# Kernel tuning notes

Measured on AMD Instinct MI355X. Metric: run time of the kernel, lower is better.

## Reference

```python
import jax, jax.numpy as jnp
import numpy as np
import math

D_MODEL = 1024
N_HEAD = 16


def setup_inputs() -> dict:
    key = jax.random.key(0)
    ks = jax.random.split(key, 11)
    B, S, D = 2, 2048, D_MODEL
    s = 1.0 / math.sqrt(D)
    return {
        "q": jax.random.normal(ks[0], (B, S, D), dtype=jnp.float32),
        "k": jax.random.normal(ks[1], (B, S, D), dtype=jnp.float32),
        "v": jax.random.normal(ks[2], (B, S, D), dtype=jnp.float32),
        "w_q": jax.random.normal(ks[3], (D, D), dtype=jnp.float32) * s,
        "b_q": jnp.zeros((D,), dtype=jnp.float32),
        "w_k": jax.random.normal(ks[4], (D, D), dtype=jnp.float32) * s,
        "b_k": jnp.zeros((D,), dtype=jnp.float32),
        "w_v": jax.random.normal(ks[5], (D, D), dtype=jnp.float32) * s,
        "b_v": jnp.zeros((D,), dtype=jnp.float32),
        "w_out": jax.random.normal(ks[6], (D, D), dtype=jnp.float32) * s,
        "b_out": jnp.zeros((D,), dtype=jnp.float32),
    }


def _split_heads(x, n_head):
    B, S, D = x.shape
    return x.reshape(B, S, n_head, D // n_head).transpose(0, 2, 1, 3)  # [B,H,S,dk]


def reference(q, k, v, w_q, b_q, w_k, b_k, w_v, b_v, w_out, b_out):
    # Linear projections (weights stored as [in, out])
    qh = _split_heads(q @ w_q + b_q, N_HEAD)
    kh = _split_heads(k @ w_k + b_k, N_HEAD)
    vh = _split_heads(v @ w_v + b_v, N_HEAD)
    d_k = qh.shape[-1]
    scores = jnp.einsum("bhqd,bhkd->bhqk", qh, kh) / jnp.sqrt(jnp.float32(d_k))
    attn = jax.nn.softmax(scores, axis=-1)
    context = jnp.einsum("bhqk,bhkd->bhqd", attn, vh)  # [B,H,S,dk]
    B, H, S, dk = context.shape
    context = context.transpose(0, 2, 1, 3).reshape(B, S, H * dk)
    return context @ w_out + b_out
```

## Files before the change

### kernel.cpp

```cpp
#include <hip/hip_runtime.h>
#include <hip/hip_bf16.h>


typedef __bf16 bf16x8 __attribute__((ext_vector_type(8)));
typedef float  f32x4  __attribute__((ext_vector_type(4)));

#define DEVI __device__ __forceinline__
#define SWZ(row, cb) ((cb) ^ (((row) & 7) << 4))

#define GLOAD16(gsrc, ldst)                                                    \
    __builtin_amdgcn_global_load_lds(                                          \
        (const __attribute__((address_space(1))) unsigned int*)(gsrc),         \
        (__attribute__((address_space(3))) unsigned int*)(ldst), 16, 0, 0)

#define BAR()        asm volatile("s_barrier" ::: "memory")
#define WAIT_LGKM0() asm volatile("s_waitcnt lgkmcnt(0)" ::: "memory")
#define WAIT_VM0()   asm volatile("s_waitcnt vmcnt(0)" ::: "memory")
#define WAIT_VM4()   asm volatile("s_waitcnt vmcnt(4)" ::: "memory")

static DEVI unsigned short f2bf(float f) {
    __hip_bfloat16 h = __float2bfloat16(f);
    return __builtin_bit_cast(unsigned short, h);
}
static DEVI unsigned int pack2(float a, float b) {
    return (unsigned int)f2bf(a) | ((unsigned int)f2bf(b) << 16);
}
static DEVI bf16x8 ldsRead(const char* p) {
    return __builtin_bit_cast(bf16x8, *(const uint4*)p);
}

__global__ __launch_bounds__(256) void wtrans_kernel(
    const float* w0, const float* w1, const float* w2, const float* w3,
    unsigned short* t0, unsigned short* t1, unsigned short* t2, unsigned short* t3)
{
    __shared__ unsigned short tile[64][80];
    const int z = blockIdx.z;
    const float* w = (z == 0) ? w0 : (z == 1) ? w1 : (z == 2) ? w2 : w3;
    unsigned short* wt = (z == 0) ? t0 : (z == 1) ? t1 : (z == 2) ? t2 : t3;
    const int n0 = blockIdx.x * 64, k0 = blockIdx.y * 64;
    const int t = threadIdx.x;
#pragma unroll
    for (int i = 0; i < 4; i++) {
        int chunk = t + i * 256;
        int row = chunk >> 4, c4 = chunk & 15;
        float4 v = *(const float4*)(w + (size_t)(k0 + row) * 1024 + n0 + c4 * 4);
        tile[c4 * 4 + 0][row] = f2bf(v.x);
        tile[c4 * 4 + 1][row] = f2bf(v.y);
        tile[c4 * 4 + 2][row] = f2bf(v.z);
        tile[c4 * 4 + 3][row] = f2bf(v.w);
    }
    __syncthreads();
#pragma unroll
    for (int i = 0; i < 2; i++) {
        int idx = t + i * 256;
        int row = idx >> 3, ch = idx & 7;
        uint4 vv = *(const uint4*)(&tile[row][ch * 8]);
        *(uint4*)(wt + (size_t)(n0 + row) * 1024 + k0 + ch * 8) = vv;
    }
}

__global__ __launch_bounds__(256, 3) void gemm_proj_kernel(
    const float* x0, const float* x1, const float* x2,
    const unsigned short* wt0, const unsigned short* wt1, const unsigned short* wt2,
    const float* b0, const float* b1, const float* b2,
    unsigned short* y0, unsigned short* y1, unsigned short* y2)
{
    __shared__ __align__(16) char Af[32768];
    __shared__ __align__(16) char Bs[16384];
    const int i = blockIdx.x;
    const int xcd = i & 7, j = i >> 3;
    const int panel = xcd * 12 + (j >> 3);
    const int z = panel >> 5, mblk = panel & 31;
    const int n0 = (j & 7) * 128, m0 = mblk * 128;

    const float* X = (z == 0) ? x0 : (z == 1) ? x1 : x2;
    const unsigned short* Wt = (z == 0) ? wt0 : (z == 1) ? wt1 : wt2;
    const float* bias = (z == 0) ? b0 : (z == 1) ? b1 : b2;
    unsigned short* Y = (z == 0) ? y0 : (z == 1) ? y1 : y2;
    const float scale = (z == 0) ? 0.125f * 1.44269504f : 1.0f;
    const int t = threadIdx.x, w = t >> 6, l = t & 63, l15 = l & 15, l4 = l >> 4;
    const int wr = w >> 1, wc = w & 1;
    const char* Ab = (const char*)X;
    const char* Bb = (const char*)Wt;

    f32x4 acc[4][4];
#pragma unroll
    for (int mr = 0; mr < 4; mr++)
#pragma unroll
        for (int nc = 0; nc < 4; nc++) acc[mr][nc] = f32x4{0.f, 0.f, 0.f, 0.f};

#pragma unroll 1
    for (int k = 0; k < 16; ++k) {
        const int k0 = k * 64;
        BAR();
#pragma unroll
        for (int jj = 0; jj < 8; jj++) {
            int o = w * 8192 + jj * 1024 + l * 16;
            int row = o >> 8, cb = (o >> 4) & 15;
            int csw = cb ^ ((row & 7) << 1);
            GLOAD16(Ab + ((size_t)(m0 + row) * 1024 + k0 + csw * 4) * 4,
                    Af + w * 8192 + jj * 1024);
        }
#pragma unroll
        for (int jj = 0; jj < 4; jj++) {
            int o = w * 4096 + jj * 1024 + l * 16;
            int row = o >> 7, cb = (o >> 4) & 7;
            int csw = cb ^ (row & 7);
            GLOAD16(Bb + ((size_t)(n0 + row) * 1024 + k0 + csw * 8) * 2,
                    Bs + w * 4096 + jj * 1024);
        }
        WAIT_VM0();
        BAR();

        bf16x8 af[4][2], bfr[4][2];
#pragma unroll
        for (int mr = 0; mr < 4; mr++) {
            int row = wr * 64 + mr * 16 + l15;
            int x = (row & 7) << 1;
#pragma unroll
            for (int kf = 0; kf < 2; kf++) {
                int cb = kf * 8 + l4 * 2;
                const char* p = Af + row * 256 + (cb ^ x) * 16;
                float4 a = *(const float4*)p;
                float4 b = *(const float4*)(p + 16);
                uint4 pk = {pack2(a.x, a.y), pack2(a.z, a.w),
                            pack2(b.x, b.y), pack2(b.z, b.w)};
                af[mr][kf] = __builtin_bit_cast(bf16x8, pk);
            }
        }
#pragma unroll
        for (int nc = 0; nc < 4; nc++) {
            int row = wc * 64 + nc * 16 + l15;
#pragma unroll
            for (int kf = 0; kf < 2; kf++)
                bfr[nc][kf] = ldsRead(Bs + row * 128 + SWZ(row, kf * 64 + l4 * 16));
        }
        __builtin_amdgcn_s_setprio(1);
#pragma unroll
        for (int kf = 0; kf < 2; kf++)
#pragma unroll
            for (int mr = 0; mr < 4; mr++)
#pragma unroll
                for (int nc = 0; nc < 4; nc++)
                    acc[mr][nc] = __builtin_amdgcn_mfma_f32_16x16x32_bf16(
                        af[mr][kf], bfr[nc][kf], acc[mr][nc], 0, 0, 0);
        __builtin_amdgcn_s_setprio(0);
    }

    WAIT_LGKM0();
    BAR();
    char* Es = Af;
    if (z < 2) {
#pragma unroll
        for (int nc = 0; nc < 4; nc++) {
            float bv = bias[n0 + wc * 64 + nc * 16 + l15];
#pragma unroll
            for (int mr = 0; mr < 4; mr++)
#pragma unroll
                for (int r = 0; r < 4; r++) {
                    int mloc = wr * 64 + mr * 16 + l4 * 4 + r;
                    int nloc = wc * 64 + nc * 16 + l15;
                    *(unsigned short*)(Es + mloc * 256 + nloc * 2) =
                        f2bf((acc[mr][nc][r] + bv) * scale);
                }
        }
        WAIT_LGKM0();
        BAR();
#pragma unroll
        for (int ii = 0; ii < 8; ii++) {
            int idx = t + ii * 256, row = idx >> 4, ch = idx & 15;
            *(uint4*)((char*)Y + ((size_t)(m0 + row) * 1024 + n0 + ch * 8) * 2) =
                *(const uint4*)(Es + row * 256 + ch * 16);
        }
    } else {
#pragma unroll
        for (int nc = 0; nc < 4; nc++) {
            float bv = bias[n0 + wc * 64 + nc * 16 + l15];
#pragma unroll
            for (int mr = 0; mr < 4; mr++)
#pragma unroll
                for (int r = 0; r < 4; r++) {
                    int mloc = wr * 64 + mr * 16 + l4 * 4 + r;
                    int nloc = wc * 64 + nc * 16 + l15;
                    *(unsigned short*)(Es + nloc * 256 + mloc * 2) =
                        f2bf(acc[mr][nc][r] + bv);
                }
        }
        WAIT_LGKM0();
        BAR();
        const int bb = m0 >> 11, s0 = m0 & 2047;
#pragma unroll
        for (int ii = 0; ii < 8; ii++) {
            int idx = t + ii * 256, row = idx >> 4, ch = idx & 15;
            int col = n0 + row, h = col >> 6, d = col & 63;
            *(uint4*)((char*)Y +
                      (((size_t)((bb * 16 + h) * 64 + d)) * 2048 + s0 + ch * 8) * 2) =
                *(const uint4*)(Es + row * 256 + ch * 16);
        }
    }
}

__global__ __launch_bounds__(256, 4) void attn_kernel(
    const unsigned short* Q2, const unsigned short* K2, const unsigned short* VT,
    unsigned short* ctx)
{
    __shared__ __align__(16) char sm[40960];
    char* QPs = sm;
    char* K0s = sm + 8192;
    char* K1s = sm + 16384;
    char* V0s = sm + 24576;
    char* V1s = sm + 32768;
    const int t = threadIdx.x, w = t >> 6, l = t & 63, l15 = l & 15, l4 = l >> 4;
    char* Ps = QPs + w * 2048;

    const int i = blockIdx.x;
    const int xcd = i & 7, j = i >> 3;
    const int bh = xcd * 4 + (j >> 5), qblk = j & 31;
    const int b = bh >> 4, h = bh & 15;
    const int q0 = qblk * 64;
    const int t0 = qblk;
    const char* Qb = (const char*)(Q2 + ((size_t)(b * 2048 + q0)) * 1024 + h * 64);
    const char* Kb = (const char*)(K2 + ((size_t)(b * 2048)) * 1024 + h * 64);
    const char* Vb = (const char*)(VT + (size_t)bh * 64 * 2048);

    int kGO[2], vGO[2];
#pragma unroll
    for (int jj = 0; jj < 2; jj++) {
        int row = w * 16 + jj * 8 + (l >> 3);
        int ch = (l & 7) ^ (row & 7);
        kGO[jj] = row * 2048 + ch * 16;
        vGO[jj] = row * 4096 + ch * 16;
    }
    int kRO[4][2], vRO[4][2];
#pragma unroll
    for (int cc = 0; cc < 4; cc++) {
        int row = cc * 16 + l15;
#pragma unroll
        for (int kf = 0; kf < 2; kf++) {
            kRO[cc][kf] = row * 128 + SWZ(row, kf * 64 + l4 * 16);
            vRO[cc][kf] = kRO[cc][kf];
        }
    }
    int pWO[4], pRO[2];
#pragma unroll
    for (int cc = 0; cc < 4; cc++) {
        int c = (cc * 2 + (l4 >> 1)) ^ (l15 & 7);
        pWO[cc] = l15 * 128 + c * 16 + (l4 & 1) * 8;
    }
#pragma unroll
    for (int kf = 0; kf < 2; kf++)
        pRO[kf] = l15 * 128 + SWZ(l15, kf * 64 + l4 * 16);

#define STAGE_KV(TT, Kdst, Vdst)                                               \
    do {                                                                       \
        int kk0 = (TT) * 64;                                                   \
        _Pragma("unroll") for (int jj = 0; jj < 2; jj++) {                     \
            GLOAD16(Kb + (size_t)(kk0 * 2048 + kGO[jj]),                       \
                    (Kdst) + w * 2048 + jj * 1024);                            \
            GLOAD16(Vb + (size_t)(kk0 * 2 + vGO[jj]),                          \
                    (Vdst) + w * 2048 + jj * 1024);                            \
        }                                                                      \
    } while (0)

    STAGE_KV(t0, K0s, V0s);

#pragma unroll
    for (int ii = 0; ii < 2; ii++) {
        int idx = t + ii * 256, row = idx >> 3, ch = idx & 7;
        uint4 vv = *(const uint4*)(Qb + (size_t)row * 2048 + ch * 16);
        *(uint4*)(QPs + row * 128 + SWZ(row, ch * 16)) = vv;
    }
    WAIT_LGKM0();
    BAR();
    bf16x8 qf[2];
    {
        int row = w * 16 + l15;
#pragma unroll
        for (int kf = 0; kf < 2; kf++)
            qf[kf] = ldsRead(QPs + row * 128 + SWZ(row, kf * 64 + l4 * 16));
    }
    WAIT_LGKM0();
    BAR();

    bf16x8 ones;
#pragma unroll
    for (int e = 0; e < 8; e++) ones[e] = (__bf16)1.0f;

    f32x4 o[4], ol;
#pragma unroll
    for (int c = 0; c < 4; c++) o[c] = f32x4{0.f, 0.f, 0.f, 0.f};
    ol = f32x4{0.f, 0.f, 0.f, 0.f};

#pragma unroll 1
    for (int it = 0; it < 32; it++) {
        char* Kc = (it & 1) ? K1s : K0s;
        char* Vc = (it & 1) ? V1s : V0s;
        char* Kn = (it & 1) ? K0s : K1s;
        char* Vn = (it & 1) ? V0s : V1s;
        if (it < 31) {
            STAGE_KV((t0 + it + 1) & 31, Kn, Vn);
            WAIT_VM4();
        } else {
            WAIT_VM0();
        }
        BAR();

        f32x4 sacc[4];
#pragma unroll
        for (int c = 0; c < 4; c++) sacc[c] = f32x4{0.f, 0.f, 0.f, 0.f};
        __builtin_amdgcn_s_setprio(1);
#pragma unroll
        for (int cc = 0; cc < 4; cc++)
#pragma unroll
            for (int kf = 0; kf < 2; kf++) {
                bf16x8 kfrag = ldsRead(Kc + kRO[cc][kf]);
                sacc[cc] = __builtin_amdgcn_mfma_f32_16x16x32_bf16(kfrag, qf[kf], sacc[cc], 0, 0, 0);
            }
        __builtin_amdgcn_s_setprio(0);

#pragma unroll
        for (int cc = 0; cc < 4; cc++)
#pragma unroll
            for (int r = 0; r < 4; r++) sacc[cc][r] = exp2f(sacc[cc][r]);

#pragma unroll
        for (int cc = 0; cc < 4; cc++) {
            uint2 pk = {pack2(sacc[cc][0], sacc[cc][1]), pack2(sacc[cc][2], sacc[cc][3])};
            *(uint2*)(Ps + pWO[cc]) = pk;
        }
        asm volatile("" ::: "memory");
        bf16x8 pf[2];
#pragma unroll
        for (int kf = 0; kf < 2; kf++)
            pf[kf] = ldsRead(Ps + pRO[kf]);

        __builtin_amdgcn_s_setprio(1);
#pragma unroll
        for (int dd = 0; dd < 4; dd++)
#pragma unroll
            for (int kf = 0; kf < 2; kf++) {
                bf16x8 vfrag = ldsRead(Vc + vRO[dd][kf]);
                o[dd] = __builtin_amdgcn_mfma_f32_16x16x32_bf16(vfrag, pf[kf], o[dd], 0, 0, 0);
            }
#pragma unroll
        for (int kf = 0; kf < 2; kf++)
            ol = __builtin_amdgcn_mfma_f32_16x16x32_bf16(ones, pf[kf], ol, 0, 0, 0);
        __builtin_amdgcn_s_setprio(0);

        WAIT_LGKM0();
        BAR();
    }
#undef STAGE_KV

    float rinv = 1.0f / ol[0];
    int q = q0 + w * 16 + l15;
    unsigned short* crow = ctx + ((size_t)(b * 2048 + q)) * 1024 + h * 64;
#pragma unroll
    for (int dd = 0; dd < 4; dd++) {
        uint2 pk = {pack2(o[dd][0] * rinv, o[dd][1] * rinv),
                    pack2(o[dd][2] * rinv, o[dd][3] * rinv)};
        *(uint2*)(crow + dd * 16 + l4 * 4) = pk;
    }
}

__global__ __launch_bounds__(256, 3) void gemm_out_kernel(
    const unsigned short* ctx, const unsigned short* wto, const float* bias, float* out)
{
    __shared__ __align__(16) char As[16384];
    __shared__ __align__(16) char Bs[16384];
    const int i = blockIdx.x;
    const int xcd = i & 7, j = i >> 3;
    const int mpanel = xcd * 4 + (j >> 3);
    const int n0 = (j & 7) * 128, m0 = mpanel * 128;
    const int t = threadIdx.x, w = t >> 6, l = t & 63, l15 = l & 15, l4 = l >> 4;
    const int wr = w >> 1, wc = w & 1;
    const char* Ab = (const char*)ctx;
    const char* Bb = (const char*)wto;

    f32x4 acc[4][4];
#pragma unroll
    for (int mr = 0; mr < 4; mr++)
#pragma unroll
        for (int nc = 0; nc < 4; nc++) acc[mr][nc] = f32x4{0.f, 0.f, 0.f, 0.f};

#pragma unroll 1
    for (int k = 0; k < 16; ++k) {
        const int k0 = k * 64;
        BAR();
#pragma unroll
        for (int jj = 0; jj < 4; jj++) {
            int o = w * 4096 + jj * 1024 + l * 16;
            int row = o >> 7, cb = (o >> 4) & 7;
            int csw = cb ^ (row & 7);
            GLOAD16(Ab + ((size_t)(m0 + row) * 1024 + k0 + csw * 8) * 2,
                    As + w * 4096 + jj * 1024);
        }
#pragma unroll
        for (int jj = 0; jj < 4; jj++) {
            int o = w * 4096 + jj * 1024 + l * 16;
            int row = o >> 7, cb = (o >> 4) & 7;
            int csw = cb ^ (row & 7);
            GLOAD16(Bb + ((size_t)(n0 + row) * 1024 + k0 + csw * 8) * 2,
                    Bs + w * 4096 + jj * 1024);
        }
        WAIT_VM0();
        BAR();

        bf16x8 af[4][2], bfr[4][2];
#pragma unroll
        for (int mr = 0; mr < 4; mr++) {
            int row = wr * 64 + mr * 16 + l15;
#pragma unroll
            for (int kf = 0; kf < 2; kf++)
                af[mr][kf] = ldsRead(As + row * 128 + SWZ(row, kf * 64 + l4 * 16));
        }
#pragma unroll
        for (int nc = 0; nc < 4; nc++) {
            int row = wc * 64 + nc * 16 + l15;
#pragma unroll
            for (int kf = 0; kf < 2; kf++)
                bfr[nc][kf] = ldsRead(Bs + row * 128 + SWZ(row, kf * 64 + l4 * 16));
        }
        __builtin_amdgcn_s_setprio(1);
#pragma unroll
        for (int kf = 0; kf < 2; kf++)
#pragma unroll
            for (int mr = 0; mr < 4; mr++)
#pragma unroll
                for (int nc = 0; nc < 4; nc++)
                    acc[mr][nc] = __builtin_amdgcn_mfma_f32_16x16x32_bf16(
                        af[mr][kf], bfr[nc][kf], acc[mr][nc], 0, 0, 0);
        __builtin_amdgcn_s_setprio(0);
    }

#pragma unroll
    for (int nc = 0; nc < 4; nc++) {
        int col = n0 + wc * 64 + nc * 16 + l15;
        float bv = bias[col];
#pragma unroll
        for (int mr = 0; mr < 4; mr++)
#pragma unroll
            for (int r = 0; r < 4; r++) {
                int m = m0 + wr * 64 + mr * 16 + l4 * 4 + r;
                out[(size_t)m * 1024 + col] = acc[mr][nc][r] + bv;
            }
    }
}

extern "C" void kernel_launch(void* const* d_in, const int* in_sizes, int n_in,
                              void* d_out, int out_size, void* d_ws, size_t ws_size,
                              hipStream_t stream)
{
    (void)in_sizes; (void)n_in; (void)out_size; (void)ws_size;
    const float* q  = (const float*)d_in[0];
    const float* k  = (const float*)d_in[1];
    const float* v  = (const float*)d_in[2];
    const float* wq = (const float*)d_in[3];
    const float* bq = (const float*)d_in[4];
    const float* wk = (const float*)d_in[5];
    const float* bk = (const float*)d_in[6];
    const float* wv = (const float*)d_in[7];
    const float* bv = (const float*)d_in[8];
    const float* wo = (const float*)d_in[9];
    const float* bo = (const float*)d_in[10];

    char* ws = (char*)d_ws;
    const size_t MB = 1u << 20;
    unsigned short* WTq = (unsigned short*)(ws + 0 * MB);
    unsigned short* WTk = (unsigned short*)(ws + 2 * MB);
    unsigned short* WTv = (unsigned short*)(ws + 4 * MB);
    unsigned short* WTo = (unsigned short*)(ws + 6 * MB);
    unsigned short* Q2  = (unsigned short*)(ws + 8 * MB);
    unsigned short* K2  = (unsigned short*)(ws + 16 * MB);
    unsigned short* VT  = (unsigned short*)(ws + 24 * MB);
    unsigned short* CTX = (unsigned short*)(ws + 32 * MB);

    wtrans_kernel<<<dim3(16, 16, 4), 256, 0, stream>>>(wq, wk, wv, wo, WTq, WTk, WTv, WTo);
    gemm_proj_kernel<<<768, 256, 0, stream>>>(q, k, v, WTq, WTk, WTv,
                                              bq, bk, bv, Q2, K2, VT);
    attn_kernel<<<1024, 256, 0, stream>>>(Q2, K2, VT, CTX);
    gemm_out_kernel<<<256, 256, 0, stream>>>(CTX, WTo, bo, (float*)d_out);
}
```

Baseline: 142.5 us.

## Process two 16-row query tiles per wave to reuse K/V fragments

Doubles the attention block's query tile from 64 to 128 rows, so each wave handles two 16-row query sub-tiles. Each K and V fragment read from LDS now feeds two MFMAs, and K/V global staging is amortized over twice as many queries, halving the grid to 512 blocks. The cost is more registers, more LDS (48KB) and lower occupancy (launch bounds 3), plus fewer blocks to cover the CUs. The softmax still uses exp2 without a running max, unchanged from before.

```diff
diff --git a/kernel.cpp b/kernel.cpp
--- a/kernel.cpp
+++ b/kernel.cpp
@@ -200,25 +200,25 @@
     }
 }
 
-__global__ __launch_bounds__(256, 4) void attn_kernel(
+__global__ __launch_bounds__(256, 3) void attn_kernel(
     const unsigned short* Q2, const unsigned short* K2, const unsigned short* VT,
     unsigned short* ctx)
 {
-    __shared__ __align__(16) char sm[40960];
+    __shared__ __align__(16) char sm[49152];
     char* QPs = sm;
-    char* K0s = sm + 8192;
-    char* K1s = sm + 16384;
-    char* V0s = sm + 24576;
-    char* V1s = sm + 32768;
+    char* K0s = sm + 16384;
+    char* K1s = sm + 24576;
+    char* V0s = sm + 32768;
+    char* V1s = sm + 40960;
     const int t = threadIdx.x, w = t >> 6, l = t & 63, l15 = l & 15, l4 = l >> 4;
-    char* Ps = QPs + w * 2048;
+    char* Ps = QPs + w * 4096;
 
     const int i = blockIdx.x;
     const int xcd = i & 7, j = i >> 3;
-    const int bh = xcd * 4 + (j >> 5), qblk = j & 31;
+    const int bh = xcd * 4 + (j >> 4), qblk = j & 15;
     const int b = bh >> 4, h = bh & 15;
-    const int q0 = qblk * 64;
-    const int t0 = qblk;
+    const int q0 = qblk * 128;
+    const int t0 = (qblk * 2) & 31;
     const char* Qb = (const char*)(Q2 + ((size_t)(b * 2048 + q0)) * 1024 + h * 64);
     const char* Kb = (const char*)(K2 + ((size_t)(b * 2048)) * 1024 + h * 64);
     const char* Vb = (const char*)(VT + (size_t)bh * 64 * 2048);
@@ -231,25 +231,27 @@
         kGO[jj] = row * 2048 + ch * 16;
         vGO[jj] = row * 4096 + ch * 16;
     }
-    int kRO[4][2], vRO[4][2];
+    int kRO[4][2];
 #pragma unroll
     for (int cc = 0; cc < 4; cc++) {
         int row = cc * 16 + l15;
 #pragma unroll
-        for (int kf = 0; kf < 2; kf++) {
+        for (int kf = 0; kf < 2; kf++)
             kRO[cc][kf] = row * 128 + SWZ(row, kf * 64 + l4 * 16);
-            vRO[cc][kf] = kRO[cc][kf];
-        }
-    }
-    int pWO[4], pRO[2];
-#pragma unroll
-    for (int cc = 0; cc < 4; cc++) {
-        int c = (cc * 2 + (l4 >> 1)) ^ (l15 & 7);
-        pWO[cc] = l15 * 128 + c * 16 + (l4 & 1) * 8;
-    }
-#pragma unroll
-    for (int kf = 0; kf < 2; kf++)
-        pRO[kf] = l15 * 128 + SWZ(l15, kf * 64 + l4 * 16);
+    }
+    int pWO[2][4], pRO[2][2];
+#pragma unroll
+    for (int qi = 0; qi < 2; qi++) {
+        int row = qi * 16 + l15;
+#pragma unroll
+        for (int cc = 0; cc < 4; cc++) {
+            int c = (cc * 2 + (l4 >> 1)) ^ (l15 & 7);
+            pWO[qi][cc] = row * 128 + c * 16 + (l4 & 1) * 8;
+        }
+#pragma unroll
+        for (int kf = 0; kf < 2; kf++)
+            pRO[qi][kf] = row * 128 + SWZ(row, kf * 64 + l4 * 16);
+    }
 
 #define STAGE_KV(TT, Kdst, Vdst)                                               \
     do {                                                                       \
@@ -265,19 +267,20 @@
     STAGE_KV(t0, K0s, V0s);
 
 #pragma unroll
-    for (int ii = 0; ii < 2; ii++) {
+    for (int ii = 0; ii < 4; ii++) {
         int idx = t + ii * 256, row = idx >> 3, ch = idx & 7;
         uint4 vv = *(const uint4*)(Qb + (size_t)row * 2048 + ch * 16);
         *(uint4*)(QPs + row * 128 + SWZ(row, ch * 16)) = vv;
     }
     WAIT_LGKM0();
     BAR();
-    bf16x8 qf[2];
-    {
-        int row = w * 16 + l15;
+    bf16x8 qf[2][2];
+#pragma unroll
+    for (int qi = 0; qi < 2; qi++) {
+        int row = w * 32 + qi * 16 + l15;
 #pragma unroll
         for (int kf = 0; kf < 2; kf++)
-            qf[kf] = ldsRead(QPs + row * 128 + SWZ(row, kf * 64 + l4 * 16));
+            qf[qi][kf] = ldsRead(QPs + row * 128 + SWZ(row, kf * 64 + l4 * 16));
     }
     WAIT_LGKM0();
     BAR();
@@ -286,10 +289,13 @@
 #pragma unroll
     for (int e = 0; e < 8; e++) ones[e] = (__bf16)1.0f;
 
-    f32x4 o[4], ol;
-#pragma unroll
-    for (int c = 0; c < 4; c++) o[c] = f32x4{0.f, 0.f, 0.f, 0.f};
-    ol = f32x4{0.f, 0.f, 0.f, 0.f};
+    f32x4 o[2][4], ol[2];
+#pragma unroll
+    for (int qi = 0; qi < 2; qi++) {
+#pragma unroll
+        for (int c = 0; c < 4; c++) o[qi][c] = f32x4{0.f, 0.f, 0.f, 0.f};
+        ol[qi] = f32x4{0.f, 0.f, 0.f, 0.f};
+    }
 
 #pragma unroll 1
     for (int it = 0; it < 32; it++) {
@@ -305,46 +311,64 @@
         }
         BAR();
 
-        f32x4 sacc[4];
-#pragma unroll
-        for (int c = 0; c < 4; c++) sacc[c] = f32x4{0.f, 0.f, 0.f, 0.f};
+        f32x4 sacc[2][4];
+#pragma unroll
+        for (int qi = 0; qi < 2; qi++)
+#pragma unroll
+            for (int c = 0; c < 4; c++) sacc[qi][c] = f32x4{0.f, 0.f, 0.f, 0.f};
         __builtin_amdgcn_s_setprio(1);
 #pragma unroll
         for (int cc = 0; cc < 4; cc++)
 #pragma unroll
             for (int kf = 0; kf < 2; kf++) {
                 bf16x8 kfrag = ldsRead(Kc + kRO[cc][kf]);
-                sacc[cc] = __builtin_amdgcn_mfma_f32_16x16x32_bf16(kfrag, qf[kf], sacc[cc], 0, 0, 0);
+#pragma unroll
+                for (int qi = 0; qi < 2; qi++)
+                    sacc[qi][cc] = __builtin_amdgcn_mfma_f32_16x16x32_bf16(
+                        kfrag, qf[qi][kf], sacc[qi][cc], 0, 0, 0);
             }
         __builtin_amdgcn_s_setprio(0);
 
 #pragma unroll
-        for (int cc = 0; cc < 4; cc++)
-#pragma unroll
-            for (int r = 0; r < 4; r++) sacc[cc][r] = exp2f(sacc[cc][r]);
-
-#pragma unroll
-        for (int cc = 0; cc < 4; cc++) {
-            uint2 pk = {pack2(sacc[cc][0], sacc[cc][1]), pack2(sacc[cc][2], sacc[cc][3])};
-            *(uint2*)(Ps + pWO[cc]) = pk;
-        }
+        for (int qi = 0; qi < 2; qi++)
+#pragma unroll
+            for (int cc = 0; cc < 4; cc++)
+#pragma unroll
+                for (int r = 0; r < 4; r++) sacc[qi][cc][r] = exp2f(sacc[qi][cc][r]);
+
+#pragma unroll
+        for (int qi = 0; qi < 2; qi++)
+#pragma unroll
+            for (int cc = 0; cc < 4; cc++) {
+                uint2 pk = {pack2(sacc[qi][cc][0], sacc[qi][cc][1]),
+                            pack2(sacc[qi][cc][2], sacc[qi][cc][3])};
+                *(uint2*)(Ps + pWO[qi][cc]) = pk;
+            }
         asm volatile("" ::: "memory");
-        bf16x8 pf[2];
-#pragma unroll
-        for (int kf = 0; kf < 2; kf++)
-            pf[kf] = ldsRead(Ps + pRO[kf]);
+        bf16x8 pf[2][2];
+#pragma unroll
+        for (int qi = 0; qi < 2; qi++)
+#pragma unroll
+            for (int kf = 0; kf < 2; kf++)
+                pf[qi][kf] = ldsRead(Ps + pRO[qi][kf]);
 
         __builtin_amdgcn_s_setprio(1);
 #pragma unroll
         for (int dd = 0; dd < 4; dd++)
 #pragma unroll
             for (int kf = 0; kf < 2; kf++) {
-                bf16x8 vfrag = ldsRead(Vc + vRO[dd][kf]);
-                o[dd] = __builtin_amdgcn_mfma_f32_16x16x32_bf16(vfrag, pf[kf], o[dd], 0, 0, 0);
+                bf16x8 vfrag = ldsRead(Vc + kRO[dd][kf]);
+#pragma unroll
+                for (int qi = 0; qi < 2; qi++)
+                    o[qi][dd] = __builtin_amdgcn_mfma_f32_16x16x32_bf16(
+                        vfrag, pf[qi][kf], o[qi][dd], 0, 0, 0);
             }
 #pragma unroll
-        for (int kf = 0; kf < 2; kf++)
-            ol = __builtin_amdgcn_mfma_f32_16x16x32_bf16(ones, pf[kf], ol, 0, 0, 0);
+        for (int qi = 0; qi < 2; qi++)
+#pragma unroll
+            for (int kf = 0; kf < 2; kf++)
+                ol[qi] = __builtin_amdgcn_mfma_f32_16x16x32_bf16(
+                    ones, pf[qi][kf], ol[qi], 0, 0, 0);
         __builtin_amdgcn_s_setprio(0);
 
         WAIT_LGKM0();
@@ -352,14 +376,17 @@
     }
 #undef STAGE_KV
 
-    float rinv = 1.0f / ol[0];
-    int q = q0 + w * 16 + l15;
-    unsigned short* crow = ctx + ((size_t)(b * 2048 + q)) * 1024 + h * 64;
-#pragma unroll
-    for (int dd = 0; dd < 4; dd++) {
-        uint2 pk = {pack2(o[dd][0] * rinv, o[dd][1] * rinv),
-                    pack2(o[dd][2] * rinv, o[dd][3] * rinv)};
-        *(uint2*)(crow + dd * 16 + l4 * 4) = pk;
+#pragma unroll
+    for (int qi = 0; qi < 2; qi++) {
+        float rinv = 1.0f / ol[qi][0];
+        int q = q0 + w * 32 + qi * 16 + l15;
+        unsigned short* crow = ctx + ((size_t)(b * 2048 + q)) * 1024 + h * 64;
+#pragma unroll
+        for (int dd = 0; dd < 4; dd++) {
+            uint2 pk = {pack2(o[qi][dd][0] * rinv, o[qi][dd][1] * rinv),
+                        pack2(o[qi][dd][2] * rinv, o[qi][dd][3] * rinv)};
+            *(uint2*)(crow + dd * 16 + l4 * 4) = pk;
+        }
     }
 }
 
@@ -478,6 +505,6 @@
     wtrans_kernel<<<dim3(16, 16, 4), 256, 0, stream>>>(wq, wk, wv, wo, WTq, WTk, WTv, WTo);
     gemm_proj_kernel<<<768, 256, 0, stream>>>(q, k, v, WTq, WTk, WTv,
                                               bq, bk, bv, Q2, K2, VT);
-    attn_kernel<<<1024, 256, 0, stream>>>(Q2, K2, VT, CTX);
+    attn_kernel<<<512, 256, 0, stream>>>(Q2, K2, VT, CTX);
     gemm_out_kernel<<<256, 256, 0, stream>>>(CTX, WTo, bo, (float*)d_out);
 }
```

Measured after the change: 140.8 us. No clear change (-1.2%).
